# Kernel tuning notes

Hardware: AMD Instinct MI355X
Metric: run time of the kernel (lower is better)

The kernel has to match this reference:

```python
import jax, jax.numpy as jnp
import numpy as np

HIDDEN = 4096
NUM_HEADS = 32
GROUP_NUM = 8
HEAD_DIM = HIDDEN // NUM_HEADS


def setup_inputs() -> dict:
    key = jax.random.key(0)
    ks = jax.random.split(key, 9)
    s = 0.02
    kv_dim = GROUP_NUM * HEAD_DIM
    return {
        "hidden_state": jax.random.normal(ks[0], (1, 2048, HIDDEN), dtype=jnp.float32),
        "wq": jax.random.normal(ks[1], (HIDDEN, HIDDEN), dtype=jnp.float32) * s,
        "bq": jnp.zeros((HIDDEN,), dtype=jnp.float32),
        "wk": jax.random.normal(ks[2], (HIDDEN, kv_dim), dtype=jnp.float32) * s,
        "bk": jnp.zeros((kv_dim,), dtype=jnp.float32),
        "wv": jax.random.normal(ks[3], (HIDDEN, kv_dim), dtype=jnp.float32) * s,
        "bv": jnp.zeros((kv_dim,), dtype=jnp.float32),
        "wo": jax.random.normal(ks[4], (HIDDEN, HIDDEN), dtype=jnp.float32) * s,
        "bo": jnp.zeros((HIDDEN,), dtype=jnp.float32),
    }


def reference(hidden_state, wq, bq, wk, bk, wv, bv, wo, bo):
    B, S, _ = hidden_state.shape
    q = hidden_state @ wq + bq                      # [B,S,H*D]
    k = hidden_state @ wk + bk                      # [B,S,G*D]
    v = hidden_state @ wv + bv                      # [B,S,G*D]

    q = q.reshape(B, S, NUM_HEADS, HEAD_DIM).transpose(0, 2, 1, 3)   # [B,H,S,D]
    k = k.reshape(B, S, GROUP_NUM, HEAD_DIM).transpose(0, 2, 1, 3)   # [B,G,S,D]
    v = v.reshape(B, S, GROUP_NUM, HEAD_DIM).transpose(0, 2, 1, 3)
    # broadcast KV groups to all heads (repeat each group heads_per_group times)
    rep = NUM_HEADS // GROUP_NUM
    k = jnp.repeat(k, rep, axis=1)                  # [B,H,S,D]
    v = jnp.repeat(v, rep, axis=1)

    scale = 1.0 / jnp.sqrt(jnp.float32(HEAD_DIM))
    scores = jnp.einsum("bhqd,bhkd->bhqk", q, k) * scale  # [B,H,S,S]
    probs = jax.nn.softmax(scores, axis=-1)
    out = jnp.einsum("bhqk,bhkd->bhqd", probs, v)         # [B,H,S,D]
    # faithful to original: transpose(-1,-2) then view (NOT a standard head merge)
    out = jnp.swapaxes(out, -1, -2).reshape(B, -1, HEAD_DIM * NUM_HEADS)  # [B,S,H*D]
    return out @ wo + bo
```

## Files before the change

### kernel.cpp

```cpp
#include <hip/hip_runtime.h>
#include <stdint.h>

#define HIDDEN 4096
#define SEQ    2048
#define NHEADS 32
#define HDIM   128
#define KVDIM  1024

typedef __attribute__((ext_vector_type(8))) short short8;
typedef __attribute__((ext_vector_type(4))) unsigned short ushort4v;
typedef __attribute__((ext_vector_type(4))) float f32x4;
typedef __attribute__((ext_vector_type(16))) float f32x16;
typedef __attribute__((ext_vector_type(4))) float float4v;
typedef __attribute__((ext_vector_type(4))) int int4v;

__device__ __forceinline__ unsigned short f2bf(float f) {
    union { float f; unsigned u; } v; v.f = f;
    unsigned r = v.u + 0x7FFFu + ((v.u >> 16) & 1u);
    return (unsigned short)(r >> 16);
}

__device__ __forceinline__ float fexp2(float x) {
#if __has_builtin(__builtin_amdgcn_exp2f)
    return __builtin_amdgcn_exp2f(x);
#else
    return exp2f(x);
#endif
}

__global__ void cast_bf16_kernel(const float* __restrict__ in,
                                 unsigned short* __restrict__ out, int n4) {
    int i = blockIdx.x * blockDim.x + threadIdx.x;
    if (i >= n4) return;
    float4v v = *(const float4v*)(in + (size_t)i * 4);
    ushort4v o;
    o.x = f2bf(v.x); o.y = f2bf(v.y); o.z = f2bf(v.z); o.w = f2bf(v.w);
    *(ushort4v*)(out + (size_t)i * 4) = o;
}

__global__ void transpose_cast_all_kernel(const float* __restrict__ wq,
                                          const float* __restrict__ wk,
                                          const float* __restrict__ wv,
                                          const float* __restrict__ wo,
                                          unsigned short* __restrict__ wqkvt,
                                          unsigned short* __restrict__ wot) {
    __shared__ float tile[64][65];
    int cx = blockIdx.x;
    const float* src; unsigned short* dst; int C; int cxl;
    if (cx < 64)      { src = wq; dst = wqkvt; C = HIDDEN; cxl = cx; }
    else if (cx < 80) { src = wk; dst = wqkvt + (size_t)4096 * HIDDEN; C = KVDIM; cxl = cx - 64; }
    else if (cx < 96) { src = wv; dst = wqkvt + (size_t)5120 * HIDDEN; C = KVDIM; cxl = cx - 80; }
    else              { src = wo; dst = wot;   C = HIDDEN; cxl = cx - 96; }
    const int R = HIDDEN;
    int r0 = blockIdx.y << 6, c0 = cxl << 6;
    int t = threadIdx.x;
    int lr = t >> 4, lc = (t & 15) << 2;
#pragma unroll
    for (int i = 0; i < 4; i++) {
        int r = lr + i * 16;
        float4v v = *(const float4v*)(src + (size_t)(r0 + r) * C + c0 + lc);
        tile[r][lc] = v.x; tile[r][lc + 1] = v.y;
        tile[r][lc + 2] = v.z; tile[r][lc + 3] = v.w;
    }
    __syncthreads();
#pragma unroll
    for (int i = 0; i < 4; i++) {
        int c = lr + i * 16;
        ushort4v o;
        o.x = f2bf(tile[lc][c]);     o.y = f2bf(tile[lc + 1][c]);
        o.z = f2bf(tile[lc + 2][c]); o.w = f2bf(tile[lc + 3][c]);
        *(ushort4v*)(dst + (size_t)(c0 + c) * R + r0 + lc) = o;
    }
}

__device__ __forceinline__ void gload_lds16(const void* g, void* l) {
    __builtin_amdgcn_global_load_lds(
        (const __attribute__((address_space(1))) void*)g,
        (__attribute__((address_space(3))) void*)l, 16, 0, 0);
}

template <int MODE>
__global__ __launch_bounds__(512, 2)
void gemm256_kernel(const unsigned short* __restrict__ A,
                    const unsigned short* __restrict__ Bt,
                    const float* __restrict__ b0,
                    const float* __restrict__ b1,
                    const float* __restrict__ b2,
                    unsigned short* __restrict__ Qo,
                    unsigned short* __restrict__ Ko,
                    unsigned short* __restrict__ Vto,
                    float* __restrict__ Of,
                    float qscale) {
    const int K = HIDDEN;
    __shared__ __align__(16) char lds[2 * 65536];

    int t = threadIdx.x;
    int w = t >> 6, l = t & 63;
    int fr = l & 15, fq = l >> 4;
    int wm = w >> 2, wn = w & 3;

    int nwg = gridDim.x * gridDim.y;
    int orig = blockIdx.y * gridDim.x + blockIdx.x;
    int cpx = nwg >> 3;
    int swz = (orig & 7) * cpx + (orig >> 3);
    int bx = swz % gridDim.x, by = swz / gridDim.x;
    int mbase = by * 256, nbase = bx * 256;

    int rband = t >> 3;
    int ch = (t & 7) ^ (rband & 7);
    const unsigned short* pA = A + (size_t)(mbase + rband) * K + ch * 8;
    const unsigned short* pB = Bt + (size_t)(nbase + rband) * K + ch * 8;
    int wdst = w * 1024;

    int rbA[8], rbB[4], cko[2];
#pragma unroll
    for (int m = 0; m < 8; m++) rbA[m] = (wm * 128 + m * 16 + fr) * 128;
#pragma unroll
    for (int n = 0; n < 4; n++) rbB[n] = (wn * 64 + n * 16 + fr) * 128;
#pragma unroll
    for (int kk = 0; kk < 2; kk++) cko[kk] = (((kk << 2) + fq) ^ (fr & 7)) * 16;

    f32x4 acc[8][4];
    f32x4 z = {0.f, 0.f, 0.f, 0.f};
#pragma unroll
    for (int m = 0; m < 8; m++)
#pragma unroll
        for (int n = 0; n < 4; n++) acc[m][n] = z;

    const int NT = K / 64;
    const size_t K64 = (size_t)64 * K;

#define STAGE8(bufbase, ts)                                              \
    {                                                                    \
        size_t ko = (size_t)(ts) * 64;                                   \
        char* lb = lds + (bufbase);                                      \
        gload_lds16(pA + ko,            lb + wdst);                      \
        gload_lds16(pA + ko + K64,      lb + 8192 + wdst);               \
        gload_lds16(pA + ko + 2 * K64,  lb + 16384 + wdst);              \
        gload_lds16(pA + ko + 3 * K64,  lb + 24576 + wdst);              \
        gload_lds16(pB + ko,            lb + 32768 + wdst);              \
        gload_lds16(pB + ko + K64,      lb + 40960 + wdst);              \
        gload_lds16(pB + ko + 2 * K64,  lb + 49152 + wdst);              \
        gload_lds16(pB + ko + 3 * K64,  lb + 57344 + wdst);              \
    }

#define COMPUTE(bufbase)                                                          \
    {                                                                             \
        const char* _b = lds + (bufbase);                                         \
        _Pragma("unroll")                                                         \
        for (int kk = 0; kk < 2; kk++) {                                          \
            short8 af[8], bf[4];                                                  \
            _Pragma("unroll")                                                     \
            for (int m = 0; m < 8; m++)                                           \
                af[m] = *(const short8*)(_b + rbA[m] + cko[kk]);                  \
            _Pragma("unroll")                                                     \
            for (int n = 0; n < 4; n++)                                           \
                bf[n] = *(const short8*)(_b + 32768 + rbB[n] + cko[kk]);          \
            __builtin_amdgcn_s_setprio(1);                                        \
            _Pragma("unroll")                                                     \
            for (int m = 0; m < 8; m++)                                           \
                _Pragma("unroll")                                                 \
                for (int n = 0; n < 4; n++)                                       \
                    acc[m][n] = __builtin_amdgcn_mfma_f32_16x16x32_bf16(          \
                        af[m], bf[n], acc[m][n], 0, 0, 0);                        \
            __builtin_amdgcn_s_setprio(0);                                        \
        }                                                                         \
    }

    STAGE8(0, 0);
    int cb = 0;
    for (int tt = 0; tt < NT - 1; ++tt) {
        STAGE8((cb ^ 1) * 65536, tt + 1);
        __builtin_amdgcn_sched_barrier(0);
        asm volatile("s_waitcnt vmcnt(8)" ::: "memory");
        __builtin_amdgcn_s_barrier();
        __builtin_amdgcn_sched_barrier(0);
        COMPUTE(cb * 65536);
        __builtin_amdgcn_sched_barrier(0);
        __builtin_amdgcn_s_barrier();
        cb ^= 1;
    }
    asm volatile("s_waitcnt vmcnt(0)" ::: "memory");
    __builtin_amdgcn_s_barrier();
    __builtin_amdgcn_sched_barrier(0);
    COMPUTE(cb * 65536);
#undef STAGE8
#undef COMPUTE

    if (MODE == 1) {
        if (nbase < 4096) {
#pragma unroll
            for (int n = 0; n < 4; n++) {
                int col = nbase + wn * 64 + n * 16 + fr;
                float bb = b0[col];
#pragma unroll
                for (int m = 0; m < 8; m++) {
                    int row = mbase + wm * 128 + m * 16 + fq * 4;
                    unsigned short* cp = Qo + (size_t)row * HIDDEN + col;
#pragma unroll
                    for (int r = 0; r < 4; r++)
                        cp[(size_t)r * HIDDEN] = f2bf((acc[m][n][r] + bb) * qscale);
                }
            }
        } else if (nbase < 5120) {
#pragma unroll
            for (int n = 0; n < 4; n++) {
                int col = nbase - 4096 + wn * 64 + n * 16 + fr;
                float bb = b1[col];
#pragma unroll
                for (int m = 0; m < 8; m++) {
                    int row = mbase + wm * 128 + m * 16 + fq * 4;
                    unsigned short* cp = Ko + (size_t)row * KVDIM + col;
#pragma unroll
                    for (int r = 0; r < 4; r++)
                        cp[(size_t)r * KVDIM] = f2bf(acc[m][n][r] + bb);
                }
            }
        } else {
#pragma unroll
            for (int n = 0; n < 4; n++) {
                int col = nbase - 5120 + wn * 64 + n * 16 + fr;
                float bb = b2[col];
#pragma unroll
                for (int m = 0; m < 8; m++) {
                    int row = mbase + wm * 128 + m * 16 + fq * 4;
                    ushort4v o;
                    o.x = f2bf(acc[m][n][0] + bb);
                    o.y = f2bf(acc[m][n][1] + bb);
                    o.z = f2bf(acc[m][n][2] + bb);
                    o.w = f2bf(acc[m][n][3] + bb);
                    *(ushort4v*)(Vto + (size_t)col * SEQ + row) = o;
                }
            }
        }
    } else {
#pragma unroll
        for (int n = 0; n < 4; n++) {
            int col = nbase + wn * 64 + n * 16 + fr;
            float bb = b0[col];
#pragma unroll
            for (int m = 0; m < 8; m++) {
                int row = mbase + wm * 128 + m * 16 + fq * 4;
                float* cp = Of + (size_t)row * HIDDEN + col;
#pragma unroll
                for (int r = 0; r < 4; r++)
                    cp[(size_t)r * HIDDEN] = acc[m][n][r] + bb;
            }
        }
    }
}

#define SWZ(off, row) ((off) ^ (((row) & 7) << 4))
__global__ __launch_bounds__(256, 2)
void attn_kernel(const unsigned short* __restrict__ Q,
                 const unsigned short* __restrict__ Kc,
                 const unsigned short* __restrict__ Vt,
                 unsigned short* __restrict__ Mg) {
    __shared__ __align__(16) char Kb[2][64 * 256];
    __shared__ __align__(16) char Vb[2][128 * 128];
    int qb = blockIdx.x, head = blockIdx.y, g = head >> 2;
    int t = threadIdx.x, w = t >> 6, l = t & 63;
    int lq = l & 31, lh = l >> 5;

    short8 qf[8];
    {
        const unsigned short* qp =
            Q + (size_t)(qb * 128 + w * 32 + lq) * HIDDEN + head * HDIM + lh * 8;
#pragma unroll
        for (int kk = 0; kk < 8; kk++) qf[kk] = *(const short8*)(qp + kk * 16);
    }

    f32x16 accO[4];
#pragma unroll
    for (int n = 0; n < 4; n++)
#pragma unroll
        for (int r = 0; r < 16; r++) accO[n][r] = 0.f;
    float Lrun = 0.f;

    int krow = t >> 2; int kcb = (t & 3) * 64;
    int vrow = t >> 1; int vcb = (t & 1) * 64;
    const unsigned short* ksrc = Kc + (size_t)krow * KVDIM + g * HDIM + (t & 3) * 32;
    const unsigned short* vsrc = Vt + (size_t)(g * HDIM + vrow) * SEQ + (t & 1) * 32;
    int kwb = krow * 256 + kcb;
    int vwb = vrow * 128 + vcb;

    const int NT = SEQ / 64;
    short8 kreg[4], vreg[4];
#pragma unroll
    for (int j = 0; j < 4; j++) kreg[j] = *(const short8*)(ksrc + j * 8);
#pragma unroll
    for (int j = 0; j < 4; j++) vreg[j] = *(const short8*)(vsrc + j * 8);
#pragma unroll
    for (int j = 0; j < 4; j++) *(short8*)(Kb[0] + SWZ(kwb + j * 16, krow)) = kreg[j];
#pragma unroll
    for (int j = 0; j < 4; j++) *(short8*)(Vb[0] + SWZ(vwb + j * 16, vrow)) = vreg[j];
#pragma unroll
    for (int j = 0; j < 4; j++) kreg[j] = *(const short8*)(ksrc + (size_t)64 * KVDIM + j * 8);
#pragma unroll
    for (int j = 0; j < 4; j++) vreg[j] = *(const short8*)(vsrc + 64 + j * 8);

    for (int tl = 0; tl < NT; tl++) {
        int b = tl & 1;
        __syncthreads();
        if (tl + 1 < NT) {
#pragma unroll
            for (int j = 0; j < 4; j++) *(short8*)(Kb[b ^ 1] + SWZ(kwb + j * 16, krow)) = kreg[j];
#pragma unroll
            for (int j = 0; j < 4; j++) *(short8*)(Vb[b ^ 1] + SWZ(vwb + j * 16, vrow)) = vreg[j];
            if (tl + 2 < NT) {
                const unsigned short* ks = ksrc + (size_t)(tl + 2) * 64 * KVDIM;
                const unsigned short* vs = vsrc + (tl + 2) * 64;
#pragma unroll
                for (int j = 0; j < 4; j++) kreg[j] = *(const short8*)(ks + j * 8);
#pragma unroll
                for (int j = 0; j < 4; j++) vreg[j] = *(const short8*)(vs + j * 8);
            }
        }
        const char* kb = Kb[b];
        const char* vb = Vb[b];

        f32x16 s0, s1;
#pragma unroll
        for (int r = 0; r < 16; r++) { s0[r] = 0.f; s1[r] = 0.f; }
#pragma unroll
        for (int kk = 0; kk < 8; kk++) {
            int cb2 = kk * 32 + lh * 16;
            short8 kf0 = *(const short8*)(kb + SWZ(lq * 256 + cb2, lq));
            short8 kf1 = *(const short8*)(kb + SWZ((lq + 32) * 256 + cb2, lq));
            s0 = __builtin_amdgcn_mfma_f32_32x32x16_bf16(kf0, qf[kk], s0, 0, 0, 0);
            s1 = __builtin_amdgcn_mfma_f32_32x32x16_bf16(kf1, qf[kk], s1, 0, 0, 0);
        }

        float sum = 0.f;
#pragma unroll
        for (int r = 0; r < 16; r++) { s0[r] = fexp2(s0[r]); sum += s0[r]; }
#pragma unroll
        for (int r = 0; r < 16; r++) { s1[r] = fexp2(s1[r]); sum += s1[r]; }
        sum += __shfl_xor(sum, 32);
        Lrun += sum;

        int W0[8], W1[8];
#pragma unroll
        for (int i = 0; i < 8; i++)
            W0[i] = (int)((unsigned)f2bf(s0[2 * i]) | ((unsigned)f2bf(s0[2 * i + 1]) << 16));
#pragma unroll
        for (int i = 0; i < 8; i++)
            W1[i] = (int)((unsigned)f2bf(s1[2 * i]) | ((unsigned)f2bf(s1[2 * i + 1]) << 16));

        short8 pa[4];
#pragma unroll
        for (int kkp = 0; kkp < 4; kkp++) {
            int k4 = (kkp & 1) * 4;
            int o0 = (kkp < 2) ? W0[k4 + 0] : W1[k4 + 0];
            int o1 = (kkp < 2) ? W0[k4 + 1] : W1[k4 + 1];
            int o2 = (kkp < 2) ? W0[k4 + 2] : W1[k4 + 2];
            int o3 = (kkp < 2) ? W0[k4 + 3] : W1[k4 + 3];
            int Za = lh ? o0 : o2;
            int Zb = lh ? o1 : o3;
            int Xa = __shfl_xor(Za, 32);
            int Xb = __shfl_xor(Zb, 32);
            int4v pw;
            pw.x = lh ? Xa : o0;
            pw.y = lh ? Xb : o1;
            pw.z = lh ? o2 : Xa;
            pw.w = lh ? o3 : Xb;
            pa[kkp] = *(short8*)&pw;
        }

#pragma unroll
        for (int n = 0; n < 4; n++) {
            int row = n * 32 + lq;
#pragma unroll
            for (int kkp = 0; kkp < 4; kkp++) {
                short8 vf = *(const short8*)(vb + SWZ(row * 128 + kkp * 32 + lh * 16, lq));
                accO[n] = __builtin_amdgcn_mfma_f32_32x32x16_bf16(pa[kkp], vf, accO[n], 0, 0, 0);
            }
        }
    }

    float rl[16];
#pragma unroll
    for (int r = 0; r < 16; r++)
        rl[r] = 1.0f / __shfl(Lrun, (r & 3) + 8 * (r >> 2) + 4 * lh);
#pragma unroll
    for (int n = 0; n < 4; n++) {
        int d = n * 32 + lq;
        int mrow = head * 64 + (d >> 1);
#pragma unroll
        for (int g2 = 0; g2 < 4; g2++) {
            int mcol = (d & 1) * SEQ + qb * 128 + w * 32 + 8 * g2 + 4 * lh;
            ushort4v o;
            o.x = f2bf(accO[n][g2 * 4 + 0] * rl[g2 * 4 + 0]);
            o.y = f2bf(accO[n][g2 * 4 + 1] * rl[g2 * 4 + 1]);
            o.z = f2bf(accO[n][g2 * 4 + 2] * rl[g2 * 4 + 2]);
            o.w = f2bf(accO[n][g2 * 4 + 3] * rl[g2 * 4 + 3]);
            *(ushort4v*)(Mg + (size_t)mrow * HIDDEN + mcol) = o;
        }
    }
}

extern "C" void kernel_launch(void* const* d_in, const int* in_sizes, int n_in,
                              void* d_out, int out_size, void* d_ws, size_t ws_size,
                              hipStream_t stream) {
    const float* x  = (const float*)d_in[0];
    const float* wq = (const float*)d_in[1];
    const float* bq = (const float*)d_in[2];
    const float* wk = (const float*)d_in[3];
    const float* bk = (const float*)d_in[4];
    const float* wv = (const float*)d_in[5];
    const float* bv = (const float*)d_in[6];
    const float* wo = (const float*)d_in[7];
    const float* bo = (const float*)d_in[8];

    char* base = (char*)d_ws;
    unsigned short* xb     = (unsigned short*)(base + 0);
    unsigned short* wqkvt  = (unsigned short*)(base + 16777216);
    unsigned short* wot    = (unsigned short*)(base + 67108864);
    unsigned short* qbuf   = (unsigned short*)(base + 100663296);
    unsigned short* kbuf   = (unsigned short*)(base + 117440512);
    unsigned short* vtbuf  = (unsigned short*)(base + 121634816);
    unsigned short* merged = (unsigned short*)(base + 125829120);

    const float QSCALE = 0.08838834764831845f * 1.4426950408889634f;

    cast_bf16_kernel<<<(SEQ * HIDDEN / 4 + 255) / 256, 256, 0, stream>>>(x, xb, SEQ * HIDDEN / 4);
    transpose_cast_all_kernel<<<dim3(160, 64), 256, 0, stream>>>(wq, wk, wv, wo, wqkvt, wot);
    gemm256_kernel<1><<<dim3(6144 / 256, SEQ / 256), 512, 0, stream>>>(
        xb, wqkvt, bq, bk, bv, qbuf, kbuf, vtbuf, nullptr, QSCALE);
    attn_kernel<<<dim3(SEQ / 128, NHEADS), 256, 0, stream>>>(qbuf, kbuf, vtbuf, merged);
    gemm256_kernel<2><<<dim3(HIDDEN / 256, SEQ / 256), 512, 0, stream>>>(
        merged, wot, bo, nullptr, nullptr, nullptr, nullptr, nullptr, (float*)d_out, 1.0f);
}
```

Measured before the change: 363.7 us.

## Restructure GEMM main loop into four sub-tile phases with inline-asm LDS reads

```diff
diff --git a/kernel.cpp b/kernel.cpp
--- a/kernel.cpp
+++ b/kernel.cpp
@@ -79,18 +79,21 @@
         (__attribute__((address_space(3))) void*)l, 16, 0, 0);
 }
 
+#define ASM_BARRIER() asm volatile("s_barrier" ::: "memory")
+#define DSR128(dst, addr) asm volatile("ds_read_b128 %0, %1" : "=v"(dst) : "v"(addr))
+
 template <int MODE>
 __global__ __launch_bounds__(512, 2)
-void gemm256_kernel(const unsigned short* __restrict__ A,
-                    const unsigned short* __restrict__ Bt,
-                    const float* __restrict__ b0,
-                    const float* __restrict__ b1,
-                    const float* __restrict__ b2,
-                    unsigned short* __restrict__ Qo,
-                    unsigned short* __restrict__ Ko,
-                    unsigned short* __restrict__ Vto,
-                    float* __restrict__ Of,
-                    float qscale) {
+void gemm256p_kernel(const unsigned short* __restrict__ A,
+                     const unsigned short* __restrict__ Bt,
+                     const float* __restrict__ b0,
+                     const float* __restrict__ b1,
+                     const float* __restrict__ b2,
+                     unsigned short* __restrict__ Qo,
+                     unsigned short* __restrict__ Ko,
+                     unsigned short* __restrict__ Vto,
+                     float* __restrict__ Of,
+                     float qscale) {
     const int K = HIDDEN;
     __shared__ __align__(16) char lds[2 * 65536];
 
@@ -112,11 +115,13 @@
     const unsigned short* pB = Bt + (size_t)(nbase + rband) * K + ch * 8;
     int wdst = w * 1024;
 
-    int rbA[8], rbB[4], cko[2];
+    unsigned ldsbase = (unsigned)(size_t)(__attribute__((address_space(3))) char*)(void*)lds;
+
+    unsigned rbA[8], rbB[4], cko[2];
 #pragma unroll
     for (int m = 0; m < 8; m++) rbA[m] = (wm * 128 + m * 16 + fr) * 128;
 #pragma unroll
-    for (int n = 0; n < 4; n++) rbB[n] = (wn * 64 + n * 16 + fr) * 128;
+    for (int n = 0; n < 4; n++) rbB[n] = 32768 + (wn * 64 + n * 16 + fr) * 128;
 #pragma unroll
     for (int kk = 0; kk < 2; kk++) cko[kk] = (((kk << 2) + fq) ^ (fr & 7)) * 16;
 
@@ -144,48 +149,46 @@
         gload_lds16(pB + ko + 3 * K64,  lb + 57344 + wdst);              \
     }
 
-#define COMPUTE(bufbase)                                                          \
-    {                                                                             \
-        const char* _b = lds + (bufbase);                                         \
-        _Pragma("unroll")                                                         \
-        for (int kk = 0; kk < 2; kk++) {                                          \
-            short8 af[8], bf[4];                                                  \
-            _Pragma("unroll")                                                     \
-            for (int m = 0; m < 8; m++)                                           \
-                af[m] = *(const short8*)(_b + rbA[m] + cko[kk]);                  \
-            _Pragma("unroll")                                                     \
-            for (int n = 0; n < 4; n++)                                           \
-                bf[n] = *(const short8*)(_b + 32768 + rbB[n] + cko[kk]);          \
-            __builtin_amdgcn_s_setprio(1);                                        \
-            _Pragma("unroll")                                                     \
-            for (int m = 0; m < 8; m++)                                           \
-                _Pragma("unroll")                                                 \
-                for (int n = 0; n < 4; n++)                                       \
-                    acc[m][n] = __builtin_amdgcn_mfma_f32_16x16x32_bf16(          \
-                        af[m], bf[n], acc[m][n], 0, 0, 0);                        \
-            __builtin_amdgcn_s_setprio(0);                                        \
-        }                                                                         \
-    }
-
     STAGE8(0, 0);
-    int cb = 0;
-    for (int tt = 0; tt < NT - 1; ++tt) {
-        STAGE8((cb ^ 1) * 65536, tt + 1);
-        __builtin_amdgcn_sched_barrier(0);
-        asm volatile("s_waitcnt vmcnt(8)" ::: "memory");
-        __builtin_amdgcn_s_barrier();
-        __builtin_amdgcn_sched_barrier(0);
-        COMPUTE(cb * 65536);
-        __builtin_amdgcn_sched_barrier(0);
-        __builtin_amdgcn_s_barrier();
-        cb ^= 1;
-    }
     asm volatile("s_waitcnt vmcnt(0)" ::: "memory");
-    __builtin_amdgcn_s_barrier();
-    __builtin_amdgcn_sched_barrier(0);
-    COMPUTE(cb * 65536);
+    ASM_BARRIER();
+
+    for (int tt = 0; tt < NT; ++tt) {
+        unsigned bufo = ldsbase + (unsigned)((tt & 1) * 65536);
+        if (tt + 1 < NT) STAGE8(((tt + 1) & 1) * 65536, tt + 1);
+#pragma unroll
+        for (int q = 0; q < 4; q++) {
+            const int mq = (q >> 1) * 4;
+            const int nq = (q & 1) * 2;
+            short8 af[4][2], bf[2][2];
+#pragma unroll
+            for (int kk = 0; kk < 2; kk++) {
+#pragma unroll
+                for (int m4 = 0; m4 < 4; m4++)
+                    DSR128(af[m4][kk], bufo + rbA[mq + m4] + cko[kk]);
+#pragma unroll
+                for (int n2 = 0; n2 < 2; n2++)
+                    DSR128(bf[n2][kk], bufo + rbB[nq + n2] + cko[kk]);
+            }
+            ASM_BARRIER();
+            asm volatile("s_waitcnt lgkmcnt(0)" ::: "memory");
+            __builtin_amdgcn_sched_barrier(0);
+            __builtin_amdgcn_s_setprio(1);
+#pragma unroll
+            for (int kk = 0; kk < 2; kk++)
+#pragma unroll
+                for (int m4 = 0; m4 < 4; m4++)
+#pragma unroll
+                    for (int n2 = 0; n2 < 2; n2++)
+                        acc[mq + m4][nq + n2] = __builtin_amdgcn_mfma_f32_16x16x32_bf16(
+                            af[m4][kk], bf[n2][kk], acc[mq + m4][nq + n2], 0, 0, 0);
+            __builtin_amdgcn_s_setprio(0);
+            if (q == 3)
+                asm volatile("s_waitcnt vmcnt(0)" ::: "memory");
+            ASM_BARRIER();
+        }
+    }
 #undef STAGE8
-#undef COMPUTE
 
     if (MODE == 1) {
         if (nbase < 4096) {
@@ -425,9 +428,9 @@
 
     cast_bf16_kernel<<<(SEQ * HIDDEN / 4 + 255) / 256, 256, 0, stream>>>(x, xb, SEQ * HIDDEN / 4);
     transpose_cast_all_kernel<<<dim3(160, 64), 256, 0, stream>>>(wq, wk, wv, wo, wqkvt, wot);
-    gemm256_kernel<1><<<dim3(6144 / 256, SEQ / 256), 512, 0, stream>>>(
+    gemm256p_kernel<1><<<dim3(6144 / 256, SEQ / 256), 512, 0, stream>>>(
         xb, wqkvt, bq, bk, bv, qbuf, kbuf, vtbuf, nullptr, QSCALE);
     attn_kernel<<<dim3(SEQ / 128, NHEADS), 256, 0, stream>>>(qbuf, kbuf, vtbuf, merged);
-    gemm256_kernel<2><<<dim3(HIDDEN / 256, SEQ / 256), 512, 0, stream>>>(
+    gemm256p_kernel<2><<<dim3(HIDDEN / 256, SEQ / 256), 512, 0, stream>>>(
         merged, wot, bo, nullptr, nullptr, nullptr, nullptr, nullptr, (float*)d_out, 1.0f);
 }
```

Measured after the change: 408.3 us. 12.3% more time.
